# Kernel optimization log

Hardware: AMD Instinct MI355X
Metric: run time of the kernel (lower is better)

The kernel has to match this reference:

```python
import jax, jax.numpy as jnp
import numpy as np

BST_DEPTH = 10                      # tree depth
NB_SPLIT = 2 ** BST_DEPTH - 1       # 1023 internal (split) nodes
NB_NODES = 2 ** (BST_DEPTH + 1) - 1 # 2047 total nodes
N = 32768                           # batch size
IN_SIZE = 255                       # raw feature dim (dim = IN_SIZE + 1 after bias concat)


def setup_inputs() -> dict:
    key = jax.random.key(0)
    k1, k2, k3 = jax.random.split(key, 3)
    dim = IN_SIZE + 1
    X = jax.random.normal(k1, (N, IN_SIZE), dtype=jnp.float32)
    # A ~ U[0,1) as in torch.rand
    A = jax.random.uniform(k2, (NB_SPLIT, dim), dtype=jnp.float32)
    W = jax.random.normal(k3, (1, dim + NB_NODES), dtype=jnp.float32) * 0.02
    b = jnp.zeros((1,), dtype=jnp.float32)
    return {"X": X, "A": A, "W": W, "b": b}


def _latent_tree_z(x, A):
    """Equivalent of LatentTree._compute_q + clamp, unpruned.

    The torch code initializes q=1, scatters min(1, +/-XA) into children, then
    propagates parent mins down for `depth` iterations. The fixed point it
    reaches is exactly q_t = min(q_parent(t), sign_t * XA[:, parent(t)]) computed
    level by level (root q = 1), which is what we build here.
    """
    XA = x @ A.T  # [N, nb_split]
    n = x.shape[0]
    q_levels = [jnp.ones((n, 1), x.dtype)]  # root
    for l in range(1, BST_DEPTH + 1):
        t = np.arange(2 ** l - 1, 2 ** (l + 1) - 1)      # node ids at level l
        parent = (t - 1) // 2                            # split-node ids
        sign = np.where(t % 2 == 1, 1.0, -1.0).astype(np.float32)  # left:+, right:-
        e = XA[:, parent] * sign[None, :]                # edge values [N, 2^l]
        prev_off = 2 ** (l - 1) - 1
        q_parent = q_levels[-1][:, parent - prev_off]    # gather parent q
        q_levels.append(jnp.minimum(q_parent, e))
    q = jnp.concatenate(q_levels, axis=1)  # [N, nb_nodes]
    return jnp.clip(q, 0.0, 1.0)


def reference(X, A, W, b):
    # append bias column of ones
    x = jnp.concatenate([X, jnp.ones((X.shape[0], 1), X.dtype)], axis=1)
    z = _latent_tree_z(x, A)                 # [N, nb_nodes]
    xz = jnp.concatenate([x, z], axis=1)     # [N, dim + nb_nodes]
    return jax.nn.sigmoid(xz @ W.T + b)      # [N, 1]
```

## Files before the change

kernel.cpp:

```cpp
#include <hip/hip_runtime.h>

typedef __attribute__((ext_vector_type(8))) short    bf16x8;
typedef __attribute__((ext_vector_type(4))) float    f32x4;
typedef __attribute__((ext_vector_type(4))) float    float4_t;
typedef __attribute__((ext_vector_type(4))) unsigned u32x4;

constexpr int NSAMP    = 32768;
constexpr int INSZ     = 255;
constexpr int DIM      = 256;
constexpr int NSPLIT   = 1023;
constexpr int NCOL     = 1024;
constexpr int BM       = 64;
constexpr int NTHREADS = 512;
constexpr int NMT      = 4;
constexpr int NPASS    = 8;

constexpr int XA_OFF    = 32768;
constexpr int LDS_BYTES = XA_OFF + NCOL * 128;
constexpr size_t WS_NEED = (size_t)NCOL * DIM * 2;

extern __shared__ char smem[];

__device__ __forceinline__ short f2bf(float f) {
  unsigned x = __builtin_bit_cast(unsigned, f);
  x += 0x7fffu + ((x >> 16) & 1u);
  return (short)(x >> 16);
}
__device__ __forceinline__ float bfraw(unsigned hw16) {
  return __builtin_bit_cast(float, hw16 << 16);
}
__device__ __forceinline__ unsigned cvt_pk(float lo, float hi) {
  unsigned r;
  asm("v_cvt_pk_bf16_f32 %0, %1, %2" : "=v"(r) : "v"(lo), "v"(hi));
  return r;
}
__device__ __forceinline__ float clamp01(float v) {
  return fminf(fmaxf(v, 0.f), 1.f);
}

__device__ __forceinline__ int xat_sw(int node) {
  return ((node & 15) << 3) | ((node & 1) << 2);
}
__device__ __forceinline__ float xat_read(const char* __restrict__ xat, int t, int lane2) {
  unsigned hw = *(const unsigned short*)(xat + t * 128 + (lane2 ^ xat_sw(t)));
  return bfraw(hw);
}

__global__ void prep_frag(const float* __restrict__ A, const float* __restrict__ W,
                          u32x4* __restrict__ wsf)
{
  int t    = blockIdx.x * 512 + threadIdx.x;
  int lane = t & 63;
  int ks   = (t >> 6) & 7;
  int ct   = t >> 9;
  int col  = ct * 16 + (lane & 15);
  int k0   = ks * 32 + ((lane >> 4) << 3);
  const float* src = (col < NSPLIT) ? (A + col * DIM + k0) : (W + k0);
  float4_t a0 = *(const float4_t*)src;
  float4_t a1 = *(const float4_t*)(src + 4);
  u32x4 p;
  p[0] = cvt_pk(a0[0], a0[1]);
  p[1] = cvt_pk(a0[2], a0[3]);
  p[2] = cvt_pk(a1[0], a1[1]);
  p[3] = cvt_pk(a1[2], a1[3]);
  wsf[t] = p;
}

template<bool USE_WS>
__device__ __forceinline__ void load_bfr(int ct, bf16x8* dst, int lane,
                                         const u32x4* __restrict__ wsf,
                                         const float* __restrict__ A,
                                         const float* __restrict__ W)
{
  if constexpr (USE_WS) {
    const u32x4* fp = wsf + ct * 512 + lane;
#pragma unroll
    for (int ks = 0; ks < 8; ++ks)
      dst[ks] = __builtin_bit_cast(bf16x8, fp[ks * 64]);
  } else {
    int col = ct * 16 + (lane & 15);
    int k0  = (lane >> 4) << 3;
    const float* ap = (col < NSPLIT) ? (A + col * DIM) : W;
#pragma unroll
    for (int ks = 0; ks < 8; ++ks) {
      float4_t a0 = *(const float4_t*)(ap + ks * 32 + k0);
      float4_t a1 = *(const float4_t*)(ap + ks * 32 + k0 + 4);
      unsigned q0 = ((unsigned)(unsigned short)f2bf(a0[0])) | (((unsigned)(unsigned short)f2bf(a0[1])) << 16);
      unsigned q1 = ((unsigned)(unsigned short)f2bf(a0[2])) | (((unsigned)(unsigned short)f2bf(a0[3])) << 16);
      unsigned q2 = ((unsigned)(unsigned short)f2bf(a1[0])) | (((unsigned)(unsigned short)f2bf(a1[1])) << 16);
      unsigned q3 = ((unsigned)(unsigned short)f2bf(a1[2])) | (((unsigned)(unsigned short)f2bf(a1[3])) << 16);
      u32x4 p = {q0, q1, q2, q3};
      dst[ks] = __builtin_bit_cast(bf16x8, p);
    }
  }
}

template<int D>
__device__ __forceinline__ void dfs(int t, float q, float& acc,
                                    const char* __restrict__ xat, int lane2,
                                    const float* __restrict__ Wz)
{
  if constexpr (D > 1) {
    if (__ballot(q > 0.f) == 0ull) return;
  }
  float xa = xat_read(xat, t, lane2);
  float qL = fminf(q, xa);
  float qR = fminf(q, -xa);
  acc += clamp01(qL) * Wz[2 * t + 1] + clamp01(qR) * Wz[2 * t + 2];
  if constexpr (D > 1) {
    dfs<D - 1>(2 * t + 1, qL, acc, xat, lane2, Wz);
    dfs<D - 1>(2 * t + 2, qR, acc, xat, lane2, Wz);
  }
}

template<bool USE_WS>
__global__ __launch_bounds__(NTHREADS, 2)
void lt_main(const float* __restrict__ X, const float* __restrict__ A,
             const float* __restrict__ W, const float* __restrict__ Bv,
             const u32x4* __restrict__ wsf, float* __restrict__ Out)
{
  const int tid  = threadIdx.x;
  const int lane = tid & 63;
  const int wave = tid >> 6;
  const int m0   = blockIdx.x * BM;

  bf16x8 b0[8], b1[8];
  load_bfr<USE_WS>(wave, b0, lane, wsf, A, W);

  {
    const float4_t* Xt = (const float4_t*)(X + (size_t)m0 * INSZ);
#pragma unroll
    for (int i = 0; i < 8; ++i) {
      int idx = tid + i * NTHREADS;
      if (idx < 4080) {
        float4_t v = Xt[idx];
#pragma unroll
        for (int e = 0; e < 4; ++e) {
          int g   = idx * 4 + e;
          int row = g / 255;
          int col = g - row * 255;
          *(short*)(smem + (((row << 9) + (col << 1)) ^ ((row & 7) << 4))) = f2bf(v[e]);
        }
      }
    }
    if (tid < BM)
      *(short*)(smem + (((tid << 9) + (255 << 1)) ^ ((tid & 7) << 4))) = (short)0x3f80;
  }
  __syncthreads();

  bf16x8 xf[NMT][8];
#pragma unroll
  for (int mt = 0; mt < NMT; ++mt) {
    int row = mt * 16 + (lane & 15);
#pragma unroll
    for (int ks = 0; ks < 8; ++ks) {
      int kk = ks * 32 + ((lane >> 4) << 3);
      xf[mt][ks] = *(const bf16x8*)(smem + (((row << 9) + (kk << 1)) ^ ((row & 7) << 4)));
    }
  }

  char* xat = smem + XA_OFF;

#pragma unroll
  for (int p = 0; p < NPASS; ++p) {
    bf16x8* cur = (p & 1) ? b1 : b0;
    bf16x8* nxt = (p & 1) ? b0 : b1;
    if (p < NPASS - 1)
      load_bfr<USE_WS>((p + 1) * 8 + wave, nxt, lane, wsf, A, W);

    f32x4 acc[NMT];
#pragma unroll
    for (int mt = 0; mt < NMT; ++mt) acc[mt] = f32x4{0.f, 0.f, 0.f, 0.f};
#pragma unroll
    for (int ks = 0; ks < 8; ++ks) {
#pragma unroll
      for (int mt = 0; mt < NMT; ++mt)
        acc[mt] = __builtin_amdgcn_mfma_f32_16x16x32_bf16(xf[mt][ks], cur[ks], acc[mt], 0, 0, 0);
    }

    int node = (p * 8 + wave) * 16 + (lane & 15);
    int sw   = xat_sw(node);
    char* xrow = xat + node * 128;
#pragma unroll
    for (int mt = 0; mt < NMT; ++mt) {
#pragma unroll
      for (int h = 0; h < 2; ++h) {
        int s0 = mt * 16 + ((lane >> 4) << 2) + h * 2;
        unsigned lo = (unsigned short)f2bf(acc[mt][2 * h]);
        unsigned hi = (unsigned short)f2bf(acc[mt][2 * h + 1]);
        *(unsigned*)(xrow + ((s0 * 2) ^ sw)) = lo | (hi << 16);
      }
    }
  }
  __syncthreads();

  const float* Wz    = W + DIM;
  const int    lane2 = lane << 1;

  int s3 = 7 + wave;
  int a2 = (s3 - 1) >> 1;
  int a1 = (a2 - 1) >> 1;
  float q = 1.f;
  {
    float x0 = xat_read(xat, 0,  lane2); q = fminf(q, (a1 & 1) ? x0 : -x0);
    float x1 = xat_read(xat, a1, lane2); q = fminf(q, (a2 & 1) ? x1 : -x1);
    float x2 = xat_read(xat, a2, lane2); q = fminf(q, (s3 & 1) ? x2 : -x2);
  }
  float acc = 0.f;
  dfs<7>(s3, q, acc, xat, lane2, Wz);
  if (wave == 0)
    dfs<3>(0, 1.f, acc, xat, lane2, Wz);

  float* part = (float*)smem;
  part[(wave << 6) + lane] = acc;
  __syncthreads();

  if (tid < BM) {
    float sum = 0.f;
#pragma unroll
    for (int w = 0; w < 8; ++w) sum += part[(w << 6) + tid];
    float xw = xat_read(xat, 1023, tid << 1);
    float v  = sum + xw + Bv[0] + Wz[0];
    Out[m0 + tid] = 1.f / (1.f + __expf(-v));
  }
}

extern "C" void kernel_launch(void* const* d_in, const int* in_sizes, int n_in,
                              void* d_out, int out_size, void* d_ws, size_t ws_size,
                              hipStream_t stream) {
  (void)in_sizes; (void)n_in; (void)out_size;
  const float* X  = (const float*)d_in[0];
  const float* A  = (const float*)d_in[1];
  const float* W  = (const float*)d_in[2];
  const float* Bv = (const float*)d_in[3];
  float* Out = (float*)d_out;

  const bool use_ws = (d_ws != nullptr) && (ws_size >= WS_NEED);
  if (use_ws) {
    prep_frag<<<64, 512, 0, stream>>>(A, W, (u32x4*)d_ws);
    hipFuncSetAttribute(reinterpret_cast<const void*>(lt_main<true>),
                        hipFuncAttributeMaxDynamicSharedMemorySize, LDS_BYTES);
    lt_main<true><<<NSAMP / BM, NTHREADS, LDS_BYTES, stream>>>(
        X, A, W, Bv, (const u32x4*)d_ws, Out);
  } else {
    hipFuncSetAttribute(reinterpret_cast<const void*>(lt_main<false>),
                        hipFuncAttributeMaxDynamicSharedMemorySize, LDS_BYTES);
    lt_main<false><<<NSAMP / BM, NTHREADS, LDS_BYTES, stream>>>(
        X, A, W, Bv, nullptr, Out);
  }
}
```

Measured before the change: 37.44 us.

## Halve block tile to 32 rows and split subtrees across half-waves

Shrinks each workgroup to 32 samples and 256 threads, which doubles the number of blocks and halves LDS use per block. Each wave now takes two level-3 subtrees, one per half-wave, and a matching XA swizzle with a 64-byte row stride is introduced. The aim is higher occupancy and finer-grained ballot pruning in the tree walk, since each ballot now covers 32 samples, though a ballot over both half-waves still couples them. The cost is that the B fragments are loaded twice as often per sample, because every block streams the full 1024-column weight set for only 32 rows.

```diff
diff --git a/kernel.cpp b/kernel.cpp
--- a/kernel.cpp
+++ b/kernel.cpp
@@ -10,13 +10,13 @@
 constexpr int DIM      = 256;
 constexpr int NSPLIT   = 1023;
 constexpr int NCOL     = 1024;
-constexpr int BM       = 64;
-constexpr int NTHREADS = 512;
-constexpr int NMT      = 4;
-constexpr int NPASS    = 8;
-
-constexpr int XA_OFF    = 32768;
-constexpr int LDS_BYTES = XA_OFF + NCOL * 128;
+constexpr int BM       = 32;
+constexpr int NTHREADS = 256;
+constexpr int NMT      = 2;
+constexpr int NPASS    = 16;
+
+constexpr int XA_OFF    = 16384;
+constexpr int LDS_BYTES = XA_OFF + NCOL * 64;
 constexpr size_t WS_NEED = (size_t)NCOL * DIM * 2;
 
 extern __shared__ char smem[];
@@ -39,10 +39,10 @@
 }
 
 __device__ __forceinline__ int xat_sw(int node) {
-  return ((node & 15) << 3) | ((node & 1) << 2);
-}
-__device__ __forceinline__ float xat_read(const char* __restrict__ xat, int t, int lane2) {
-  unsigned hw = *(const unsigned short*)(xat + t * 128 + (lane2 ^ xat_sw(t)));
+  return ((node & 7) << 3) | (((node >> 3) & 1) << 2);
+}
+__device__ __forceinline__ float xat_read(const char* __restrict__ xat, int t, int s2) {
+  unsigned hw = *(const unsigned short*)(xat + t * 64 + (s2 ^ xat_sw(t)));
   return bfraw(hw);
 }
 
@@ -97,19 +97,19 @@
 
 template<int D>
 __device__ __forceinline__ void dfs(int t, float q, float& acc,
-                                    const char* __restrict__ xat, int lane2,
+                                    const char* __restrict__ xat, int s2,
                                     const float* __restrict__ Wz)
 {
   if constexpr (D > 1) {
     if (__ballot(q > 0.f) == 0ull) return;
   }
-  float xa = xat_read(xat, t, lane2);
+  float xa = xat_read(xat, t, s2);
   float qL = fminf(q, xa);
   float qR = fminf(q, -xa);
   acc += clamp01(qL) * Wz[2 * t + 1] + clamp01(qR) * Wz[2 * t + 2];
   if constexpr (D > 1) {
-    dfs<D - 1>(2 * t + 1, qL, acc, xat, lane2, Wz);
-    dfs<D - 1>(2 * t + 2, qR, acc, xat, lane2, Wz);
+    dfs<D - 1>(2 * t + 1, qL, acc, xat, s2, Wz);
+    dfs<D - 1>(2 * t + 2, qR, acc, xat, s2, Wz);
   }
 }
 
@@ -132,7 +132,7 @@
 #pragma unroll
     for (int i = 0; i < 8; ++i) {
       int idx = tid + i * NTHREADS;
-      if (idx < 4080) {
+      if (idx < 2040) {
         float4_t v = Xt[idx];
 #pragma unroll
         for (int e = 0; e < 4; ++e) {
@@ -166,7 +166,7 @@
     bf16x8* cur = (p & 1) ? b1 : b0;
     bf16x8* nxt = (p & 1) ? b0 : b1;
     if (p < NPASS - 1)
-      load_bfr<USE_WS>((p + 1) * 8 + wave, nxt, lane, wsf, A, W);
+      load_bfr<USE_WS>((p + 1) * 4 + wave, nxt, lane, wsf, A, W);
 
     f32x4 acc[NMT];
 #pragma unroll
@@ -178,9 +178,9 @@
         acc[mt] = __builtin_amdgcn_mfma_f32_16x16x32_bf16(xf[mt][ks], cur[ks], acc[mt], 0, 0, 0);
     }
 
-    int node = (p * 8 + wave) * 16 + (lane & 15);
+    int node = (p * 4 + wave) * 16 + (lane & 15);
     int sw   = xat_sw(node);
-    char* xrow = xat + node * 128;
+    char* xrow = xat + node * 64;
 #pragma unroll
     for (int mt = 0; mt < NMT; ++mt) {
 #pragma unroll
@@ -194,31 +194,36 @@
   }
   __syncthreads();
 
-  const float* Wz    = W + DIM;
-  const int    lane2 = lane << 1;
-
-  int s3 = 7 + wave;
-  int a2 = (s3 - 1) >> 1;
+  const float* Wz = W + DIM;
+  const int    s2 = (lane & 31) << 1;
+
+  int tr = ((lane < 32) ? 7 : 8) + 2 * wave;
+  int a2 = (tr - 1) >> 1;
   int a1 = (a2 - 1) >> 1;
   float q = 1.f;
   {
-    float x0 = xat_read(xat, 0,  lane2); q = fminf(q, (a1 & 1) ? x0 : -x0);
-    float x1 = xat_read(xat, a1, lane2); q = fminf(q, (a2 & 1) ? x1 : -x1);
-    float x2 = xat_read(xat, a2, lane2); q = fminf(q, (s3 & 1) ? x2 : -x2);
+    float x0 = xat_read(xat, 0,  s2); q = fminf(q, (a1 & 1) ? x0 : -x0);
+    float x1 = xat_read(xat, a1, s2); q = fminf(q, (a2 & 1) ? x1 : -x1);
+    float x2 = xat_read(xat, a2, s2); q = fminf(q, (tr & 1) ? x2 : -x2);
   }
   float acc = 0.f;
-  dfs<7>(s3, q, acc, xat, lane2, Wz);
-  if (wave == 0)
-    dfs<3>(0, 1.f, acc, xat, lane2, Wz);
+  dfs<7>(tr, q, acc, xat, s2, Wz);
+  if (wave == 0) {
+    float x0 = xat_read(xat, 0, s2);
+    float qh = (lane < 32) ? fminf(1.f, x0) : fminf(1.f, -x0);
+    int   ch = (lane < 32) ? 1 : 2;
+    acc += clamp01(qh) * Wz[ch];
+    dfs<2>(ch, qh, acc, xat, s2, Wz);
+  }
 
   float* part = (float*)smem;
-  part[(wave << 6) + lane] = acc;
+  part[tid] = acc;
   __syncthreads();
 
   if (tid < BM) {
     float sum = 0.f;
 #pragma unroll
-    for (int w = 0; w < 8; ++w) sum += part[(w << 6) + tid];
+    for (int j = 0; j < 8; ++j) sum += part[j * 32 + tid];
     float xw = xat_read(xat, 1023, tid << 1);
     float v  = sum + xw + Bv[0] + Wz[0];
     Out[m0 + tid] = 1.f / (1.f + __expf(-v));
```

Result: slower. 40.67 us (+8.6%).

## Double block threads, split waves by row tile and column group

Applied to the files above, without the earlier changes.

The main kernel now runs 1024 threads per block. Each wave owns one 16-row M tile and a contiguous group of 16 column tiles, instead of all four M tiles over 8 strided column tiles. The tree traversal is split across 16 waves with depth-6 subtrees below level 4, and the prep kernel launch shape is changed. The goal is more waves per CU to hide latency, but every B fragment is now loaded four times (once per M-tile wave). The tighter launch bounds may also force register spills with the double-buffered fragments.

```diff
diff --git a/kernel.cpp b/kernel.cpp
--- a/kernel.cpp
+++ b/kernel.cpp
@@ -11,9 +11,8 @@
 constexpr int NSPLIT   = 1023;
 constexpr int NCOL     = 1024;
 constexpr int BM       = 64;
-constexpr int NTHREADS = 512;
-constexpr int NMT      = 4;
-constexpr int NPASS    = 8;
+constexpr int NTHREADS = 1024;
+constexpr int NPASS    = 16;
 
 constexpr int XA_OFF    = 32768;
 constexpr int LDS_BYTES = XA_OFF + NCOL * 128;
@@ -49,7 +48,7 @@
 __global__ void prep_frag(const float* __restrict__ A, const float* __restrict__ W,
                           u32x4* __restrict__ wsf)
 {
-  int t    = blockIdx.x * 512 + threadIdx.x;
+  int t    = blockIdx.x * 128 + threadIdx.x;
   int lane = t & 63;
   int ks   = (t >> 6) & 7;
   int ct   = t >> 9;
@@ -114,7 +113,7 @@
 }
 
 template<bool USE_WS>
-__global__ __launch_bounds__(NTHREADS, 2)
+__global__ __launch_bounds__(NTHREADS, 4)
 void lt_main(const float* __restrict__ X, const float* __restrict__ A,
              const float* __restrict__ W, const float* __restrict__ Bv,
              const u32x4* __restrict__ wsf, float* __restrict__ Out)
@@ -122,15 +121,17 @@
   const int tid  = threadIdx.x;
   const int lane = tid & 63;
   const int wave = tid >> 6;
+  const int mt   = wave & 3;
+  const int cg   = wave >> 2;
   const int m0   = blockIdx.x * BM;
 
   bf16x8 b0[8], b1[8];
-  load_bfr<USE_WS>(wave, b0, lane, wsf, A, W);
+  load_bfr<USE_WS>(cg * NPASS, b0, lane, wsf, A, W);
 
   {
     const float4_t* Xt = (const float4_t*)(X + (size_t)m0 * INSZ);
 #pragma unroll
-    for (int i = 0; i < 8; ++i) {
+    for (int i = 0; i < 4; ++i) {
       int idx = tid + i * NTHREADS;
       if (idx < 4080) {
         float4_t v = Xt[idx];
@@ -148,14 +149,13 @@
   }
   __syncthreads();
 
-  bf16x8 xf[NMT][8];
-#pragma unroll
-  for (int mt = 0; mt < NMT; ++mt) {
+  bf16x8 xf[8];
+  {
     int row = mt * 16 + (lane & 15);
 #pragma unroll
     for (int ks = 0; ks < 8; ++ks) {
       int kk = ks * 32 + ((lane >> 4) << 3);
-      xf[mt][ks] = *(const bf16x8*)(smem + (((row << 9) + (kk << 1)) ^ ((row & 7) << 4)));
+      xf[ks] = *(const bf16x8*)(smem + (((row << 9) + (kk << 1)) ^ ((row & 7) << 4)));
     }
   }
 
@@ -166,30 +166,22 @@
     bf16x8* cur = (p & 1) ? b1 : b0;
     bf16x8* nxt = (p & 1) ? b0 : b1;
     if (p < NPASS - 1)
-      load_bfr<USE_WS>((p + 1) * 8 + wave, nxt, lane, wsf, A, W);
-
-    f32x4 acc[NMT];
-#pragma unroll
-    for (int mt = 0; mt < NMT; ++mt) acc[mt] = f32x4{0.f, 0.f, 0.f, 0.f};
-#pragma unroll
-    for (int ks = 0; ks < 8; ++ks) {
-#pragma unroll
-      for (int mt = 0; mt < NMT; ++mt)
-        acc[mt] = __builtin_amdgcn_mfma_f32_16x16x32_bf16(xf[mt][ks], cur[ks], acc[mt], 0, 0, 0);
-    }
-
-    int node = (p * 8 + wave) * 16 + (lane & 15);
+      load_bfr<USE_WS>(cg * NPASS + p + 1, nxt, lane, wsf, A, W);
+
+    f32x4 acc = {0.f, 0.f, 0.f, 0.f};
+#pragma unroll
+    for (int ks = 0; ks < 8; ++ks)
+      acc = __builtin_amdgcn_mfma_f32_16x16x32_bf16(xf[ks], cur[ks], acc, 0, 0, 0);
+
+    int node = (cg * NPASS + p) * 16 + (lane & 15);
     int sw   = xat_sw(node);
     char* xrow = xat + node * 128;
 #pragma unroll
-    for (int mt = 0; mt < NMT; ++mt) {
-#pragma unroll
-      for (int h = 0; h < 2; ++h) {
-        int s0 = mt * 16 + ((lane >> 4) << 2) + h * 2;
-        unsigned lo = (unsigned short)f2bf(acc[mt][2 * h]);
-        unsigned hi = (unsigned short)f2bf(acc[mt][2 * h + 1]);
-        *(unsigned*)(xrow + ((s0 * 2) ^ sw)) = lo | (hi << 16);
-      }
+    for (int h = 0; h < 2; ++h) {
+      int s0 = mt * 16 + ((lane >> 4) << 2) + h * 2;
+      unsigned lo = (unsigned short)f2bf(acc[2 * h]);
+      unsigned hi = (unsigned short)f2bf(acc[2 * h + 1]);
+      *(unsigned*)(xrow + ((s0 * 2) ^ sw)) = lo | (hi << 16);
     }
   }
   __syncthreads();
@@ -197,19 +189,21 @@
   const float* Wz    = W + DIM;
   const int    lane2 = lane << 1;
 
-  int s3 = 7 + wave;
-  int a2 = (s3 - 1) >> 1;
-  int a1 = (a2 - 1) >> 1;
+  int r  = 15 + wave;
+  int n3 = (r  - 1) >> 1;
+  int n2 = (n3 - 1) >> 1;
+  int n1 = (n2 - 1) >> 1;
   float q = 1.f;
   {
-    float x0 = xat_read(xat, 0,  lane2); q = fminf(q, (a1 & 1) ? x0 : -x0);
-    float x1 = xat_read(xat, a1, lane2); q = fminf(q, (a2 & 1) ? x1 : -x1);
-    float x2 = xat_read(xat, a2, lane2); q = fminf(q, (s3 & 1) ? x2 : -x2);
+    float x0 = xat_read(xat, 0,  lane2); q = fminf(q, (n1 & 1) ? x0 : -x0);
+    float x1 = xat_read(xat, n1, lane2); q = fminf(q, (n2 & 1) ? x1 : -x1);
+    float x2 = xat_read(xat, n2, lane2); q = fminf(q, (n3 & 1) ? x2 : -x2);
+    float x3 = xat_read(xat, n3, lane2); q = fminf(q, (r  & 1) ? x3 : -x3);
   }
   float acc = 0.f;
-  dfs<7>(s3, q, acc, xat, lane2, Wz);
+  dfs<6>(r, q, acc, xat, lane2, Wz);
   if (wave == 0)
-    dfs<3>(0, 1.f, acc, xat, lane2, Wz);
+    dfs<4>(0, 1.f, acc, xat, lane2, Wz);
 
   float* part = (float*)smem;
   part[(wave << 6) + lane] = acc;
@@ -218,7 +212,7 @@
   if (tid < BM) {
     float sum = 0.f;
 #pragma unroll
-    for (int w = 0; w < 8; ++w) sum += part[(w << 6) + tid];
+    for (int w = 0; w < 16; ++w) sum += part[(w << 6) + tid];
     float xw = xat_read(xat, 1023, tid << 1);
     float v  = sum + xw + Bv[0] + Wz[0];
     Out[m0 + tid] = 1.f / (1.f + __expf(-v));
@@ -237,7 +231,7 @@
 
   const bool use_ws = (d_ws != nullptr) && (ws_size >= WS_NEED);
   if (use_ws) {
-    prep_frag<<<64, 512, 0, stream>>>(A, W, (u32x4*)d_ws);
+    prep_frag<<<256, 128, 0, stream>>>(A, W, (u32x4*)d_ws);
     hipFuncSetAttribute(reinterpret_cast<const void*>(lt_main<true>),
                         hipFuncAttributeMaxDynamicSharedMemorySize, LDS_BYTES);
     lt_main<true><<<NSAMP / BM, NTHREADS, LDS_BYTES, stream>>>(
```

Result: slower. 51.56 us (+37.7%).
